# Optimization experiments

Measured on AMD Instinct MI355X. Metric: run time of the kernel, lower is better.

Reference implementation:

```python
import jax, jax.numpy as jnp
import numpy as np

B = 1_048_576
W = 64  # hidden width
N_FREQ = 6   # 3 dims * 6 freqs * (sin,cos) = 36
K_BLOB = 4   # one-blob bins per dim


def _freq_embed(p):
    # [B,3] -> [B,36]
    freqs = 2.0 ** jnp.arange(N_FREQ, dtype=p.dtype)
    ang = jnp.pi * p[:, :, None] * freqs  # [B,3,6]
    return jnp.concatenate([jnp.sin(ang), jnp.cos(ang)], axis=-1).reshape(p.shape[0], 3 * 2 * N_FREQ)


def _sph(d):
    # unit-square parameterization of a direction, [B,3] -> [B,2]
    d = d / (jnp.linalg.norm(d, axis=-1, keepdims=True) + 1e-8)
    u = jnp.arctan2(d[:, 1], d[:, 0]) / (2.0 * jnp.pi) + 0.5
    v = jnp.arccos(jnp.clip(d[:, 2], -1.0 + 1e-6, 1.0 - 1e-6)) / jnp.pi
    return jnp.stack([u, v], axis=-1)


def _one_blob(x, k=K_BLOB):
    # x in [0,1], [B,D] -> [B,D*k] Gaussian one-blob encoding
    centers = (jnp.arange(k, dtype=x.dtype) + 0.5) / k
    sigma = 1.0 / k
    g = jnp.exp(-0.5 * ((x[..., None] - centers) / sigma) ** 2)  # [B,D,k]
    return g.reshape(x.shape[0], -1)


def _encode(p, wi, n, alpha, beta, r):
    ones = jnp.ones((p.shape[0], 2), dtype=p.dtype)
    return jnp.concatenate([
        _freq_embed(p),                      # 36
        _one_blob(_sph(wi)),                 # 8
        _one_blob(_sph(n)),                  # 8
        _one_blob(1.0 - jnp.exp(-r)),        # 4
        alpha, beta,                         # 6
        ones,                                # 2 (implicit bias)
    ], axis=-1)                              # -> [B,64]


def _mlp(x, Ws):
    h = x
    for Wk in Ws[:-1]:
        h = jax.nn.relu(h @ Wk.T)
    return h @ Ws[-1].T  # [B,3]


def setup_inputs() -> dict:
    key = jax.random.key(0)
    ks = jax.random.split(key, 13)
    p = jax.random.normal(ks[0], (B, 3), jnp.float32)
    wi = jax.random.normal(ks[1], (B, 3), jnp.float32)
    n = jax.random.normal(ks[2], (B, 3), jnp.float32)
    alpha = jax.random.uniform(ks[3], (B, 3), jnp.float32)
    beta = jax.random.uniform(ks[4], (B, 3), jnp.float32)
    r = jax.random.uniform(ks[5], (B, 1), jnp.float32)
    s = 1.0 / np.sqrt(W)
    weights = {}
    for i in range(6):
        weights[f"W{i}"] = jax.random.normal(ks[6 + i], (W, W), jnp.float32) * s
    weights["W6"] = jax.random.normal(ks[12], (3, W), jnp.float32) * s
    return dict(p=p, wi=wi, n=n, alpha=alpha, beta=beta, r=r, **weights)


def reference(p, wi, n, alpha, beta, r, W0, W1, W2, W3, W4, W5, W6):
    x = _encode(p, wi, n, alpha, beta, r)
    out = _mlp(x, [W0, W1, W2, W3, W4, W5, W6])
    return out * (alpha + beta)  # reflectance factorization
```

## Files before the change

kernel.cpp:

```cpp
#include <hip/hip_runtime.h>


typedef _Float16 f16;
typedef f16 f16x2 __attribute__((ext_vector_type(2)));
typedef f16 f16x4 __attribute__((ext_vector_type(4)));
typedef f16 f16x8 __attribute__((ext_vector_type(8)));
typedef float f32x4 __attribute__((ext_vector_type(4)));

#define MFMA32(A, B, C) __builtin_amdgcn_mfma_f32_16x16x32_f16(A, B, C, 0, 0, 0)

static constexpr int TILES  = 4;
static constexpr int WAVES  = 8;
static constexpr int BLOCK  = WAVES * 64;
static constexpr int ROUNDS = 8;
static constexpr int SPB    = ROUNDS * 4 * 64;

static constexpr int    WUNITS   = 50;
static constexpr int    WCHUNKS  = WUNITS * 64;
static constexpr size_t WS_BYTES = (size_t)WCHUNKS * 16;
static constexpr int    LDS_WEI  = WUNITS * 1024;
static constexpr int    LDS_STG  = 4 * 4096;
static constexpr int    LDS_TOT  = LDS_WEI + LDS_STG;

__host__ __device__ __forceinline__ int tau(int x) {
    return (x & 32) + ((x & 7) >> 2) * 16 + ((x >> 3) & 3) * 4 + (x & 3);
}

__device__ __forceinline__ f16x2 pkh(float a, float b) {
    return __builtin_bit_cast(f16x2, __builtin_amdgcn_cvt_pkrtz(a, b));
}

__device__ __forceinline__ f16x4 cat22(f16x2 a, f16x2 b) {
    return __builtin_shufflevector(a, b, 0, 1, 2, 3);
}

__device__ __forceinline__ f16x8 cat44(f16x4 a, f16x4 b) {
    return __builtin_shufflevector(a, b, 0, 1, 2, 3, 4, 5, 6, 7);
}

__device__ __forceinline__ f16x4 pack4(f32x4 v) {
    return cat22(pkh(v[0], v[1]), pkh(v[2], v[3]));
}

__device__ __forceinline__ float fast_atan2_rev(float y, float x) {
    const float ax = __builtin_fabsf(x), ay = __builtin_fabsf(y);
    const float mx = fmaxf(ax, ay), mn = fminf(ax, ay);
    const float a = mn * __builtin_amdgcn_rcpf(fmaxf(mx, 1e-30f));
    const float s = a * a;
    float r = a * (0.99997726f + s * (-0.33262347f + s * (0.19354346f +
              s * (-0.11643287f + s * (0.05265332f - s * 0.01172120f)))));
    if (ay > ax) r = 1.5707963268f - r;
    if (x < 0.0f) r = 3.1415926536f - r;
    r = (y < 0.0f) ? -r : r;
    return r * 0.15915494309189535f;
}

__device__ __forceinline__ float fast_acos(float x) {
    const float ax = __builtin_fabsf(x);
    const float t = __builtin_amdgcn_sqrtf(1.0f - ax);
    const float p = t * (1.5707288f + ax * (-0.2121144f +
                    ax * (0.0742610f - ax * 0.0187293f)));
    return (x < 0.0f) ? (3.1415926536f - p) : p;
}

__device__ __forceinline__ void blob4(float x, float* out) {
    const float dx = x - 0.125f;
    const float E0 = __expf(-8.0f * dx * dx);
    const float R  = __expf(4.0f * dx);
    const float t1 = R * 0.60653066f;
    const float t2 = R * 0.22313016f;
    const float t3 = R * 0.082084999f;
    out[0] = E0;
    out[1] = E0 * t1;
    out[2] = out[1] * t2;
    out[3] = out[2] * t3;
}

__device__ __forceinline__ f16x8 make_wchunk(
    int c, const float* __restrict__ W0, const float* __restrict__ W1,
    const float* __restrict__ W2, const float* __restrict__ W3,
    const float* __restrict__ W4, const float* __restrict__ W5,
    const float* __restrict__ W6)
{
    const int lane2 = c & 63;
    const int unit  = c >> 6;
    const int q = lane2 >> 4, m = lane2 & 15;
    f16x8 v;
    if (unit < 48) {
        const int l = unit >> 3, kt = (unit & 7) >> 2, mt = unit & 3;
        const float* Ws[6] = {W0, W1, W2, W3, W4, W5};
        const float* __restrict__ Wl = Ws[l];
#pragma unroll
        for (int j = 0; j < 8; ++j) {
            const int x = kt * 32 + q * 8 + j;
            const int src = (l == 0) ? x : tau(x);
            v[j] = (f16)Wl[(mt * 16 + m) * 64 + src];
        }
    } else {
        const int kt = unit - 48;
#pragma unroll
        for (int j = 0; j < 8; ++j) {
            const int src = tau(kt * 32 + q * 8 + j);
            v[j] = (m < 3) ? (f16)W6[m * 64 + src] : (f16)0.0f;
        }
    }
    return v;
}

__global__ __launch_bounds__(256, 1) void pack_weights_kernel(
    const float* __restrict__ W0, const float* __restrict__ W1,
    const float* __restrict__ W2, const float* __restrict__ W3,
    const float* __restrict__ W4, const float* __restrict__ W5,
    const float* __restrict__ W6, f16* __restrict__ ws)
{
    const int c = (int)blockIdx.x * 256 + threadIdx.x;
    if (c >= WCHUNKS) return;
    *(f16x8*)(ws + (size_t)c * 8) = make_wchunk(c, W0, W1, W2, W3, W4, W5, W6);
}

__device__ __forceinline__ void async_ld16(const void* g, void* l) {
    __builtin_amdgcn_global_load_lds(
        (const __attribute__((address_space(1))) void*)g,
        (__attribute__((address_space(3))) void*)l,
        16, 0, 0);
}

template<int PACKED>
__global__ __launch_bounds__(BLOCK, 4) void nrc_mlp_kernel(
    const float* __restrict__ P,  const float* __restrict__ WI,
    const float* __restrict__ NV, const float* __restrict__ AL,
    const float* __restrict__ BE, const float* __restrict__ RR,
    const f16*   __restrict__ ws,
    const float* __restrict__ W0, const float* __restrict__ W1,
    const float* __restrict__ W2, const float* __restrict__ W3,
    const float* __restrict__ W4, const float* __restrict__ W5,
    const float* __restrict__ W6, float* __restrict__ Out)
{
    __shared__ __attribute__((aligned(16))) unsigned char smem[LDS_TOT];

    const int tid  = threadIdx.x;
    const int lane = tid & 63;
    const int w    = tid >> 6;
    const int q    = lane >> 4;
    const int m    = lane & 15;
    const bool producer = (w < 4);
    const int  cw  = w & 3;
    const int  blk_base = (int)blockIdx.x * SPB;

    unsigned char* const stg = smem + LDS_WEI;

    if (PACKED) {
#pragma unroll
        for (int i = 0; i < (WCHUNKS + BLOCK - 1) / BLOCK; ++i) {
            const int c = i * BLOCK + tid;
            if (c < WCHUNKS)
                async_ld16(ws + (size_t)c * 8, smem + c * 16);
        }
    } else {
#pragma unroll
        for (int i = 0; i < (WCHUNKS + BLOCK - 1) / BLOCK; ++i) {
            const int c = i * BLOCK + tid;
            if (c < WCHUNKS)
                *(f16x8*)(smem + c * 16) = make_wchunk(c, W0, W1, W2, W3, W4, W5, W6);
        }
    }

    const f16x4 zero4 = {(f16)0.0f, (f16)0.0f, (f16)0.0f, (f16)0.0f};
    const f32x4 ZF = {0.0f, 0.0f, 0.0f, 0.0f};
    unsigned char* const wb = smem + lane * 16;

    for (int r = 0; r < ROUNDS; ++r) {
        f16x2 hf[32];
        if (producer) {
            const int s = blk_base + r * 256 + cw * 64 + lane;

            float pv[3], wv[3], nv[3], av[3], bv[3];
#pragma unroll
            for (int d = 0; d < 3; ++d) {
                pv[d] = P [s * 3 + d];
                wv[d] = WI[s * 3 + d];
                nv[d] = NV[s * 3 + d];
                av[d] = AL[s * 3 + d];
                bv[d] = BE[s * 3 + d];
            }
            const float rv = RR[s];

#pragma unroll
            for (int d = 0; d < 3; ++d) {
                float sA[6], cA[6];
                const float fr = __builtin_amdgcn_fractf(pv[d] * 0.5f);
                sA[0] = __builtin_amdgcn_sinf(fr);
                cA[0] = __builtin_amdgcn_cosf(fr);
#pragma unroll
                for (int k = 1; k < 6; ++k) {
                    const float s2 = sA[k-1] * sA[k-1];
                    const float sc = sA[k-1] * cA[k-1];
                    cA[k] = fmaf(-2.0f, s2, 1.0f);
                    sA[k] = sc + sc;
                }
                hf[d * 6 + 0] = pkh(sA[0], sA[1]);
                hf[d * 6 + 1] = pkh(sA[2], sA[3]);
                hf[d * 6 + 2] = pkh(sA[4], sA[5]);
                hf[d * 6 + 3] = pkh(cA[0], cA[1]);
                hf[d * 6 + 4] = pkh(cA[2], cA[3]);
                hf[d * 6 + 5] = pkh(cA[4], cA[5]);
            }
#pragma unroll
            for (int which = 0; which < 2; ++which) {
                const float* dv = (which == 0) ? wv : nv;
                const int ho = 18 + which * 4;
                const float nr = __builtin_amdgcn_sqrtf(dv[0]*dv[0] + dv[1]*dv[1] + dv[2]*dv[2]) + 1e-8f;
                const float u  = fast_atan2_rev(dv[1], dv[0]) + 0.5f;
                float zc = dv[2] * __builtin_amdgcn_rcpf(nr);
                zc = fminf(fmaxf(zc, -1.0f + 1e-6f), 1.0f - 1e-6f);
                const float vv = fast_acos(zc) * 0.3183098861837907f;
                float ob[8];
                blob4(u,  &ob[0]);
                blob4(vv, &ob[4]);
                hf[ho + 0] = pkh(ob[0], ob[1]);
                hf[ho + 1] = pkh(ob[2], ob[3]);
                hf[ho + 2] = pkh(ob[4], ob[5]);
                hf[ho + 3] = pkh(ob[6], ob[7]);
            }
            {
                float ob[4];
                blob4(1.0f - __expf(-rv), ob);
                hf[26] = pkh(ob[0], ob[1]);
                hf[27] = pkh(ob[2], ob[3]);
            }
            hf[28] = pkh(av[0], av[1]);
            hf[29] = pkh(av[2], bv[0]);
            hf[30] = pkh(bv[1], bv[2]);
            hf[31] = pkh(1.0f, 1.0f);
        }

        f16x8 bf[TILES][2];
#pragma unroll
        for (int h = 0; h < 2; ++h) {
            __syncthreads();
            if (producer && ((lane >> 5) == h)) {
                unsigned char* const tb =
                    stg + cw * 4096 + ((lane >> 4) & 1) * 2048 + m * 128;
#pragma unroll
                for (int g = 0; g < 8; ++g) {
                    const int slot0 = (4 * g + 4 * m) & 31;
                    *(f16x8*)(tb + slot0 * 4) =
                        cat44(cat22(hf[g*4 + 0], hf[g*4 + 1]),
                              cat22(hf[g*4 + 2], hf[g*4 + 3]));
                }
            }
            __syncthreads();
            if (!producer) {
#pragma unroll
                for (int t2 = 0; t2 < 2; ++t2) {
#pragma unroll
                    for (int kt = 0; kt < 2; ++kt) {
                        const int s0 = (16 * kt + 4 * q + 4 * m) & 31;
                        bf[h * 2 + t2][kt] = *(const f16x8*)(
                            stg + cw * 4096 + t2 * 2048 + m * 128 + s0 * 4);
                    }
                }
            }
        }

        if (!producer) {
            __builtin_amdgcn_s_setprio(1);
#pragma unroll
            for (int layer = 0; layer < 6; ++layer) {
                f16x8 wa[8];
#pragma unroll
                for (int f = 0; f < 8; ++f)
                    wa[f] = *(const f16x8*)(wb + (layer * 8 + f) * 1024);

#pragma unroll
                for (int t = 0; t < TILES; ++t) {
                    f32x4 acc[4];
#pragma unroll
                    for (int mt = 0; mt < 4; ++mt) {
                        f32x4 z = MFMA32(wa[mt], bf[t][0], ZF);
                        z = MFMA32(wa[4 + mt], bf[t][1], z);
                        acc[mt] = z;
                    }
                    f16x4 pk[4];
#pragma unroll
                    for (int mt = 0; mt < 4; ++mt)
                        pk[mt] = __builtin_elementwise_max(pack4(acc[mt]), zero4);
                    bf[t][0] = cat44(pk[0], pk[1]);
                    bf[t][1] = cat44(pk[2], pk[3]);
                }
            }
            __builtin_amdgcn_s_setprio(0);
            const f16x8 w6f0 = *(const f16x8*)(wb + 48 * 1024);
            const f16x8 w6f1 = *(const f16x8*)(wb + 49 * 1024);
            const int rbase = blk_base + r * 256 + cw * 64;
            float aa[TILES][3];
#pragma unroll
            for (int t = 0; t < TILES; ++t) {
                const int s = rbase + t * 16 + m;
#pragma unroll
                for (int d = 0; d < 3; ++d)
                    aa[t][d] = AL[s * 3 + d] + BE[s * 3 + d];
            }
#pragma unroll
            for (int t = 0; t < TILES; ++t) {
                f32x4 z = MFMA32(w6f0, bf[t][0], ZF);
                z = MFMA32(w6f1, bf[t][1], z);
                if (lane < 16) {
                    const int s = rbase + t * 16 + m;
                    float* o = Out + s * 3;
                    o[0] = z[0] * aa[t][0];
                    o[1] = z[1] * aa[t][1];
                    o[2] = z[2] * aa[t][2];
                }
            }
        }
    }
}

extern "C" void kernel_launch(void* const* d_in, const int* in_sizes, int n_in,
                              void* d_out, int out_size, void* d_ws, size_t ws_size,
                              hipStream_t stream) {
    (void)n_in; (void)out_size;
    const float* P  = (const float*)d_in[0];
    const float* WI = (const float*)d_in[1];
    const float* NV = (const float*)d_in[2];
    const float* AL = (const float*)d_in[3];
    const float* BE = (const float*)d_in[4];
    const float* RR = (const float*)d_in[5];
    const float* W0 = (const float*)d_in[6];
    const float* W1 = (const float*)d_in[7];
    const float* W2 = (const float*)d_in[8];
    const float* W3 = (const float*)d_in[9];
    const float* W4 = (const float*)d_in[10];
    const float* W5 = (const float*)d_in[11];
    const float* W6 = (const float*)d_in[12];
    f16*   ws  = (f16*)d_ws;
    float* Out = (float*)d_out;

    const int Bn = in_sizes[0] / 3;
    const int grid = Bn / SPB;

    if (ws_size >= WS_BYTES) {
        hipLaunchKernelGGL(pack_weights_kernel, dim3((WCHUNKS + 255) / 256),
                           dim3(256), 0, stream, W0, W1, W2, W3, W4, W5, W6, ws);
        hipLaunchKernelGGL((nrc_mlp_kernel<1>), dim3(grid), dim3(BLOCK), 0, stream,
                           P, WI, NV, AL, BE, RR, ws,
                           W0, W1, W2, W3, W4, W5, W6, Out);
    } else {
        hipLaunchKernelGGL((nrc_mlp_kernel<0>), dim3(grid), dim3(BLOCK), 0, stream,
                           P, WI, NV, AL, BE, RR, ws,
                           W0, W1, W2, W3, W4, W5, W6, Out);
    }
}
```

Baseline: 179.5 us.

## Software-pipeline producer encoding with consumer MLP across rounds using paired waves

Restructures the block from 8 waves (4 producers, 4 consumers, both phases in lockstep) to 4 waves organized as 2 producer/consumer pairs. Producers encode round r while consumers run the MLP on round r-1 from staging LDS, with an epilogue for the last round. This targets the serialization where consumers idled during encoding and producers idled during MFMA work. In exchange, blocks are smaller with fewer waves per CU (launch bounds 2) and there are more rounds with barriers, so latency hiding may suffer.

```diff
diff --git a/kernel.cpp b/kernel.cpp
--- a/kernel.cpp
+++ b/kernel.cpp
@@ -10,16 +10,17 @@
 #define MFMA32(A, B, C) __builtin_amdgcn_mfma_f32_16x16x32_f16(A, B, C, 0, 0, 0)
 
 static constexpr int TILES  = 4;
-static constexpr int WAVES  = 8;
+static constexpr int WAVES  = 4;
 static constexpr int BLOCK  = WAVES * 64;
-static constexpr int ROUNDS = 8;
-static constexpr int SPB    = ROUNDS * 4 * 64;
+static constexpr int PAIRS  = 2;
+static constexpr int ROUNDS = 16;
+static constexpr int SPB    = ROUNDS * PAIRS * 64;
 
 static constexpr int    WUNITS   = 50;
 static constexpr int    WCHUNKS  = WUNITS * 64;
 static constexpr size_t WS_BYTES = (size_t)WCHUNKS * 16;
 static constexpr int    LDS_WEI  = WUNITS * 1024;
-static constexpr int    LDS_STG  = 4 * 4096;
+static constexpr int    LDS_STG  = PAIRS * 8192;
 static constexpr int    LDS_TOT  = LDS_WEI + LDS_STG;
 
 __host__ __device__ __forceinline__ int tau(int x) {
@@ -126,7 +127,7 @@
 }
 
 template<int PACKED>
-__global__ __launch_bounds__(BLOCK, 4) void nrc_mlp_kernel(
+__global__ __launch_bounds__(BLOCK, 2) void nrc_mlp_kernel(
     const float* __restrict__ P,  const float* __restrict__ WI,
     const float* __restrict__ NV, const float* __restrict__ AL,
     const float* __restrict__ BE, const float* __restrict__ RR,
@@ -143,11 +144,11 @@
     const int w    = tid >> 6;
     const int q    = lane >> 4;
     const int m    = lane & 15;
-    const bool producer = (w < 4);
-    const int  cw  = w & 3;
+    const bool producer = (w < PAIRS);
+    const int  pr  = producer ? w : (w - PAIRS);
     const int  blk_base = (int)blockIdx.x * SPB;
 
-    unsigned char* const stg = smem + LDS_WEI;
+    unsigned char* const stg = smem + LDS_WEI + pr * 8192;
 
     if (PACKED) {
 #pragma unroll
@@ -172,7 +173,7 @@
     for (int r = 0; r < ROUNDS; ++r) {
         f16x2 hf[32];
         if (producer) {
-            const int s = blk_base + r * 256 + cw * 64 + lane;
+            const int s = blk_base + r * (PAIRS * 64) + pr * 64 + lane;
 
             float pv[3], wv[3], nv[3], av[3], bv[3];
 #pragma unroll
@@ -232,86 +233,145 @@
             hf[29] = pkh(av[2], bv[0]);
             hf[30] = pkh(bv[1], bv[2]);
             hf[31] = pkh(1.0f, 1.0f);
-        }
-
-        f16x8 bf[TILES][2];
-#pragma unroll
-        for (int h = 0; h < 2; ++h) {
-            __syncthreads();
-            if (producer && ((lane >> 5) == h)) {
-                unsigned char* const tb =
-                    stg + cw * 4096 + ((lane >> 4) & 1) * 2048 + m * 128;
-#pragma unroll
-                for (int g = 0; g < 8; ++g) {
-                    const int slot0 = (4 * g + 4 * m) & 31;
-                    *(f16x8*)(tb + slot0 * 4) =
-                        cat44(cat22(hf[g*4 + 0], hf[g*4 + 1]),
-                              cat22(hf[g*4 + 2], hf[g*4 + 3]));
-                }
-            }
-            __syncthreads();
-            if (!producer) {
-#pragma unroll
-                for (int t2 = 0; t2 < 2; ++t2) {
+        } else {
+            if (r > 0) {
+                const int rr = r - 1;
+                f16x8 bf[TILES][2];
+#pragma unroll
+                for (int t = 0; t < TILES; ++t) {
 #pragma unroll
                     for (int kt = 0; kt < 2; ++kt) {
                         const int s0 = (16 * kt + 4 * q + 4 * m) & 31;
-                        bf[h * 2 + t2][kt] = *(const f16x8*)(
-                            stg + cw * 4096 + t2 * 2048 + m * 128 + s0 * 4);
+                        bf[t][kt] = *(const f16x8*)(
+                            stg + t * 2048 + m * 128 + s0 * 4);
                     }
                 }
-            }
-        }
-
-        if (!producer) {
-            __builtin_amdgcn_s_setprio(1);
-#pragma unroll
-            for (int layer = 0; layer < 6; ++layer) {
-                f16x8 wa[8];
-#pragma unroll
-                for (int f = 0; f < 8; ++f)
-                    wa[f] = *(const f16x8*)(wb + (layer * 8 + f) * 1024);
-
+                const int rbase = blk_base + rr * (PAIRS * 64) + pr * 64;
+                float aa[TILES][3];
 #pragma unroll
                 for (int t = 0; t < TILES; ++t) {
-                    f32x4 acc[4];
-#pragma unroll
-                    for (int mt = 0; mt < 4; ++mt) {
-                        f32x4 z = MFMA32(wa[mt], bf[t][0], ZF);
-                        z = MFMA32(wa[4 + mt], bf[t][1], z);
-                        acc[mt] = z;
+                    const int s = rbase + t * 16 + m;
+#pragma unroll
+                    for (int d = 0; d < 3; ++d)
+                        aa[t][d] = AL[s * 3 + d] + BE[s * 3 + d];
+                }
+
+                __builtin_amdgcn_s_setprio(1);
+#pragma unroll
+                for (int layer = 0; layer < 6; ++layer) {
+                    f16x8 wa[8];
+#pragma unroll
+                    for (int f = 0; f < 8; ++f)
+                        wa[f] = *(const f16x8*)(wb + (layer * 8 + f) * 1024);
+
+#pragma unroll
+                    for (int t = 0; t < TILES; ++t) {
+                        f32x4 acc[4];
+#pragma unroll
+                        for (int mt = 0; mt < 4; ++mt) {
+                            f32x4 z = MFMA32(wa[mt], bf[t][0], ZF);
+                            z = MFMA32(wa[4 + mt], bf[t][1], z);
+                            acc[mt] = z;
+                        }
+                        f16x4 pk[4];
+#pragma unroll
+                        for (int mt = 0; mt < 4; ++mt)
+                            pk[mt] = __builtin_elementwise_max(pack4(acc[mt]), zero4);
+                        bf[t][0] = cat44(pk[0], pk[1]);
+                        bf[t][1] = cat44(pk[2], pk[3]);
                     }
-                    f16x4 pk[4];
-#pragma unroll
-                    for (int mt = 0; mt < 4; ++mt)
-                        pk[mt] = __builtin_elementwise_max(pack4(acc[mt]), zero4);
-                    bf[t][0] = cat44(pk[0], pk[1]);
-                    bf[t][1] = cat44(pk[2], pk[3]);
-                }
-            }
-            __builtin_amdgcn_s_setprio(0);
-            const f16x8 w6f0 = *(const f16x8*)(wb + 48 * 1024);
-            const f16x8 w6f1 = *(const f16x8*)(wb + 49 * 1024);
-            const int rbase = blk_base + r * 256 + cw * 64;
-            float aa[TILES][3];
+                }
+                __builtin_amdgcn_s_setprio(0);
+                const f16x8 w6f0 = *(const f16x8*)(wb + 48 * 1024);
+                const f16x8 w6f1 = *(const f16x8*)(wb + 49 * 1024);
+#pragma unroll
+                for (int t = 0; t < TILES; ++t) {
+                    f32x4 z = MFMA32(w6f0, bf[t][0], ZF);
+                    z = MFMA32(w6f1, bf[t][1], z);
+                    if (lane < 16) {
+                        const int s = rbase + t * 16 + m;
+                        float* o = Out + s * 3;
+                        o[0] = z[0] * aa[t][0];
+                        o[1] = z[1] * aa[t][1];
+                        o[2] = z[2] * aa[t][2];
+                    }
+                }
+            }
+        }
+
+        __syncthreads();
+
+        if (producer) {
+            unsigned char* const tb = stg + (lane >> 4) * 2048 + m * 128;
+#pragma unroll
+            for (int g = 0; g < 8; ++g) {
+                const int slot0 = (4 * g + 4 * m) & 31;
+                *(f16x8*)(tb + slot0 * 4) =
+                    cat44(cat22(hf[g*4 + 0], hf[g*4 + 1]),
+                          cat22(hf[g*4 + 2], hf[g*4 + 3]));
+            }
+        }
+
+        __syncthreads();
+    }
+
+    if (!producer) {
+        const int rr = ROUNDS - 1;
+        f16x8 bf[TILES][2];
+#pragma unroll
+        for (int t = 0; t < TILES; ++t) {
+#pragma unroll
+            for (int kt = 0; kt < 2; ++kt) {
+                const int s0 = (16 * kt + 4 * q + 4 * m) & 31;
+                bf[t][kt] = *(const f16x8*)(stg + t * 2048 + m * 128 + s0 * 4);
+            }
+        }
+        const int rbase = blk_base + rr * (PAIRS * 64) + pr * 64;
+        float aa[TILES][3];
+#pragma unroll
+        for (int t = 0; t < TILES; ++t) {
+            const int s = rbase + t * 16 + m;
+#pragma unroll
+            for (int d = 0; d < 3; ++d)
+                aa[t][d] = AL[s * 3 + d] + BE[s * 3 + d];
+        }
+        __builtin_amdgcn_s_setprio(1);
+#pragma unroll
+        for (int layer = 0; layer < 6; ++layer) {
+            f16x8 wa[8];
+#pragma unroll
+            for (int f = 0; f < 8; ++f)
+                wa[f] = *(const f16x8*)(wb + (layer * 8 + f) * 1024);
 #pragma unroll
             for (int t = 0; t < TILES; ++t) {
+                f32x4 acc[4];
+#pragma unroll
+                for (int mt = 0; mt < 4; ++mt) {
+                    f32x4 z = MFMA32(wa[mt], bf[t][0], ZF);
+                    z = MFMA32(wa[4 + mt], bf[t][1], z);
+                    acc[mt] = z;
+                }
+                f16x4 pk[4];
+#pragma unroll
+                for (int mt = 0; mt < 4; ++mt)
+                    pk[mt] = __builtin_elementwise_max(pack4(acc[mt]), zero4);
+                bf[t][0] = cat44(pk[0], pk[1]);
+                bf[t][1] = cat44(pk[2], pk[3]);
+            }
+        }
+        __builtin_amdgcn_s_setprio(0);
+        const f16x8 w6f0 = *(const f16x8*)(wb + 48 * 1024);
+        const f16x8 w6f1 = *(const f16x8*)(wb + 49 * 1024);
+#pragma unroll
+        for (int t = 0; t < TILES; ++t) {
+            f32x4 z = MFMA32(w6f0, bf[t][0], ZF);
+            z = MFMA32(w6f1, bf[t][1], z);
+            if (lane < 16) {
                 const int s = rbase + t * 16 + m;
-#pragma unroll
-                for (int d = 0; d < 3; ++d)
-                    aa[t][d] = AL[s * 3 + d] + BE[s * 3 + d];
-            }
-#pragma unroll
-            for (int t = 0; t < TILES; ++t) {
-                f32x4 z = MFMA32(w6f0, bf[t][0], ZF);
-                z = MFMA32(w6f1, bf[t][1], z);
-                if (lane < 16) {
-                    const int s = rbase + t * 16 + m;
-                    float* o = Out + s * 3;
-                    o[0] = z[0] * aa[t][0];
-                    o[1] = z[1] * aa[t][1];
-                    o[2] = z[2] * aa[t][2];
-                }
+                float* o = Out + s * 3;
+                o[0] = z[0] * aa[t][0];
+                o[1] = z[1] * aa[t][1];
+                o[2] = z[2] * aa[t][2];
             }
         }
     }
```

Measured after the change: 177.1 us. About the same (-1.3%).
